# Kernel tuning notes

Measured on AMD Instinct MI355X. Metric: run time of the kernel, lower is better.

The kernel has to match this reference:

```python
import jax, jax.numpy as jnp
import numpy as np

B, H, L, N = 16, 256, 4096, 64  # N = d_state//2 retained complex-conjugate modes (S4D)
EPS = 1e-5


def setup_inputs() -> dict:
    key = jax.random.key(0)
    ks = jax.random.split(key, 6)
    x = jax.random.normal(ks[0], (B, H, L), dtype=jnp.float32)
    # dt log-uniform in [1e-3, 1e-1] per channel (standard S4 init)
    log_dt = (jax.random.uniform(ks[1], (H,), dtype=jnp.float32)
              * (np.log(0.1) - np.log(0.001)) + np.log(0.001))
    # S4D-Lin init: A_n = -1/2 + i*pi*n
    A_re = -0.5 * jnp.ones((H, N), dtype=jnp.float32)
    A_im = jnp.pi * jnp.broadcast_to(jnp.arange(N, dtype=jnp.float32), (H, N))
    # bidirectional -> 2 channel groups of C
    C_re = jax.random.normal(ks[2], (2, H, N), dtype=jnp.float32)
    C_im = jax.random.normal(ks[3], (2, H, N), dtype=jnp.float32)
    D = jax.random.normal(ks[4], (H,), dtype=jnp.float32)
    ln_w = jnp.ones((H,), dtype=jnp.float32)
    ln_b = jnp.zeros((H,), dtype=jnp.float32)
    W_out = jax.random.normal(ks[5], (H, H), dtype=jnp.float32) / np.sqrt(H)
    b_out = jnp.zeros((H,), dtype=jnp.float32)
    return {"x": x, "log_dt": log_dt, "A_re": A_re, "A_im": A_im,
            "C_re": C_re, "C_im": C_im, "D": D,
            "ln_w": ln_w, "ln_b": ln_b, "W_out": W_out, "b_out": b_out}


def _s4_forward(x, log_dt, A_re, A_im, C_re, C_im, D, ln_w, ln_b, W_out, b_out):
    # LayerNorm over channel dim (x.transpose -> LN(d_model) -> transpose back)
    mu = jnp.mean(x, axis=1, keepdims=True)
    var = jnp.mean((x - mu) ** 2, axis=1, keepdims=True)
    z = (x - mu) * jax.lax.rsqrt(var + EPS) * ln_w[None, :, None] + ln_b[None, :, None]

    # --- S4D kernel via Vandermonde (ZOH-style discretization) ---
    A = A_re + 1j * A_im                         # (H, N)
    C = C_re + 1j * C_im                         # (2, H, N)
    dt = jnp.exp(log_dt)[:, None]                # (H, 1)
    dtA = dt * A                                 # (H, N)
    C_t = C * (jnp.exp(dtA) - 1.0) / A           # (2, H, N)
    t = jnp.arange(L, dtype=jnp.float32)
    V = jnp.exp(dtA[:, :, None] * t)             # (H, N, L) Vandermonde
    K = 2.0 * jnp.real(jnp.einsum('dhn,hnl->dhl', C_t, V))  # (2, H, L)

    # bidirectional: forward kernel padded right, backward kernel flipped, padded left
    k = jnp.pad(K[0], ((0, 0), (0, L))) + jnp.pad(K[1][:, ::-1], ((0, 0), (L, 0)))

    # FFT convolution over length 2L
    Uf = jnp.fft.rfft(z, n=2 * L)                # (B, H, L+1)
    Kf = jnp.fft.rfft(k, n=2 * L)                # (H, L+1)
    y = jnp.fft.irfft(Uf * Kf[None], n=2 * L)[..., :L]

    y = y + D[None, :, None] * z                 # skip D*u
    y = jax.nn.gelu(y)                           # S4 default activation
    # transposed position-wise output linear (postact=None -> plain Linear)
    y = jnp.einsum('oh,bhl->bol', W_out, y) + b_out[None, :, None]
    return x + y                                  # residual


def reference(x, log_dt, A_re, A_im, C_re, C_im, D, ln_w, ln_b, W_out, b_out):
    return _s4_forward(x, log_dt, A_re, A_im, C_re, C_im, D, ln_w, ln_b, W_out, b_out)
```

## Files before the change

kernel.cpp:

```cpp
#include <hip/hip_runtime.h>
#include <math.h>

#define B_ 16
#define H_ 256
#define L_ 4096
#define N_ 64
#define HN (H_*N_)
#define HL (H_*L_)
#define BHL (B_*H_*L_)
#define SPAD 64

#define WVT_OFS 0
#define TM_OFS  8192
#define E2T_OFS 12288
#define MATS_PER 20480

typedef short bf16x8 __attribute__((ext_vector_type(8)));
typedef float f32x4  __attribute__((ext_vector_type(4)));

__device__ __forceinline__ unsigned int pk2(float a, float b) {
    return ((__float_as_uint(a) + 0x8000u) >> 16) |
           ((__float_as_uint(b) + 0x8000u) & 0xffff0000u);
}
__device__ __forceinline__ unsigned short bfr(float a) {
    return (unsigned short)((__float_as_uint(a) + 0x8000u) >> 16);
}
__device__ __forceinline__ float ubf(unsigned short u) {
    return __uint_as_float(((unsigned int)u) << 16);
}

__global__ void __launch_bounds__(64) mats_kernel(const float* __restrict__ log_dt,
                                                  const float* __restrict__ A_re,
                                                  const float* __restrict__ A_im,
                                                  const float* __restrict__ C_re,
                                                  const float* __restrict__ C_im,
                                                  unsigned short* __restrict__ mats,
                                                  float2* __restrict__ Wc) {
    int hd = blockIdx.x;
    int h = hd >> 1, d = hd & 1;
    int m = threadIdx.x;
    __shared__ float2 pws[65 * 64];
    __shared__ float2 c2s[64];
    __shared__ float  Karr[64];

    int i = h * 64 + m;
    float dt = expf(log_dt[h]);
    float Are = A_re[i], Aim = A_im[i];
    float dr = dt * Are, di = dt * Aim;
    float er = expf(dr);
    float wr = er * cosf(di), wi = er * sinf(di);
    float em1r = wr - 1.0f, em1i = wi;
    float inv = 1.0f / (Are * Are + Aim * Aim);
    float qr = (em1r * Are + em1i * Aim) * inv;
    float qi = (em1i * Are - em1r * Aim) * inv;
    float Cr = C_re[d * HN + i], Ci = C_im[d * HN + i];
    float2 c2;
    c2.x = 2.0f * (Cr * qr - Ci * qi);
    c2.y = 2.0f * (Cr * qi + Ci * qr);
    c2s[m] = c2;
    float pr = 1.0f, pi = 0.0f;
    for (int k = 0; k < 64; ++k) {
        float2 p; p.x = pr; p.y = pi;
        pws[k * 64 + ((m + k) & 63)] = p;
        float t = pr * wr - pi * wi;
        pi = pr * wi + pi * wr;
        pr = t;
    }
    {
        float2 p; p.x = pr; p.y = pi;
        pws[64 * 64 + ((m + 64) & 63)] = p;
        Wc[hd * 64 + m] = p;
    }
    __syncthreads();
    {
        float kk = 0.f;
        for (int mm = 0; mm < 64; ++mm) {
            float2 c = c2s[mm];
            float2 pw = pws[m * 64 + ((mm + m) & 63)];
            kk += c.x * pw.x - c.y * pw.y;
        }
        Karr[m] = kk;
    }
    __syncthreads();
    unsigned short* mb = mats + (size_t)hd * MATS_PER;
    for (int i2 = 0; i2 < 32; ++i2) {
        int e0 = 2 * i2, e1 = e0 + 1;
        int k0 = d ? e0 : 63 - e0;
        int k1 = d ? e1 : 63 - e1;
        float2 p0 = pws[k0 * 64 + ((m + k0) & 63)];
        float2 p1 = pws[k1 * 64 + ((m + k1) & 63)];
        *(unsigned int*)(mb + WVT_OFS + (2 * m) * 64 + e0)     = pk2(p0.x, p1.x);
        *(unsigned int*)(mb + WVT_OFS + (2 * m + 1) * 64 + e0) = pk2(p0.y, p1.y);
    }
    for (int i2 = 0; i2 < 32; ++i2) {
        int e0 = 2 * i2, e1 = e0 + 1;
        float v0, v1;
        if (d == 0) {
            v0 = (e0 <= m) ? Karr[m - e0] : 0.f;
            v1 = (e1 <= m) ? Karr[m - e1] : 0.f;
        } else {
            v0 = (e0 > m) ? Karr[e0 - m - 1] : 0.f;
            v1 = (e1 > m) ? Karr[e1 - m - 1] : 0.f;
        }
        *(unsigned int*)(mb + TM_OFS + m * 64 + e0) = pk2(v0, v1);
    }
    {
        int kp = d ? (63 - m) : (m + 1);
        for (int mm = 0; mm < 64; ++mm) {
            float2 c = c2s[mm];
            float2 pw = pws[kp * 64 + ((mm + kp) & 63)];
            float vr = c.x * pw.x - c.y * pw.y;
            float vi = -(c.x * pw.y + c.y * pw.x);
            *(unsigned int*)(mb + E2T_OFS + m * 128 + 2 * mm) = pk2(vr, vi);
        }
    }
}

__global__ void __launch_bounds__(256) wbf_kernel(const float* __restrict__ W,
                                                  unsigned short* __restrict__ Wbf) {
    int i = (blockIdx.x * 256 + threadIdx.x) * 4;
    float4 v = *(const float4*)(W + i);
    uint2 u;
    u.x = pk2(v.x, v.y);
    u.y = pk2(v.z, v.w);
    *(uint2*)(Wbf + i) = u;
}

__global__ void __launch_bounds__(256) ln_kernel(const float* __restrict__ x,
                                                 const float* __restrict__ lnw,
                                                 const float* __restrict__ lnb,
                                                 unsigned short* __restrict__ zb) {
    int b  = blockIdx.y;
    int l0 = blockIdx.x * 256;
    int t  = threadIdx.x;
    int hq = t >> 6, lo = t & 63;
    int l  = l0 + lo * 4;
    __shared__ float4 r1[4][64];
    __shared__ float4 r2[4][64];
    __shared__ float4 muS[64];
    __shared__ float4 rsS[64];
    const float* xb = x + (size_t)b * HL;
    float4 s1 = {0.f,0.f,0.f,0.f}, s2 = {0.f,0.f,0.f,0.f};
    #pragma unroll 4
    for (int hh = 0; hh < 64; ++hh) {
        int h = hq * 64 + hh;
        float4 v = *(const float4*)(xb + (size_t)h * L_ + l);
        s1.x += v.x; s1.y += v.y; s1.z += v.z; s1.w += v.w;
        s2.x += v.x*v.x; s2.y += v.y*v.y; s2.z += v.z*v.z; s2.w += v.w*v.w;
    }
    r1[hq][lo] = s1; r2[hq][lo] = s2;
    __syncthreads();
    if (t < 64) {
        float4 S1 = r1[0][t], S2 = r2[0][t];
        #pragma unroll
        for (int q = 1; q < 4; ++q) {
            float4 a = r1[q][t], c = r2[q][t];
            S1.x += a.x; S1.y += a.y; S1.z += a.z; S1.w += a.w;
            S2.x += c.x; S2.y += c.y; S2.z += c.z; S2.w += c.w;
        }
        const float invH = 1.0f / 256.0f;
        float4 mu, rs;
        mu.x = S1.x*invH; mu.y = S1.y*invH; mu.z = S1.z*invH; mu.w = S1.w*invH;
        rs.x = rsqrtf(S2.x*invH - mu.x*mu.x + 1e-5f);
        rs.y = rsqrtf(S2.y*invH - mu.y*mu.y + 1e-5f);
        rs.z = rsqrtf(S2.z*invH - mu.z*mu.z + 1e-5f);
        rs.w = rsqrtf(S2.w*invH - mu.w*mu.w + 1e-5f);
        muS[t] = mu; rsS[t] = rs;
    }
    __syncthreads();
    float4 mu = muS[lo], rs = rsS[lo];
    #pragma unroll 4
    for (int hh = 0; hh < 64; ++hh) {
        int h = hq * 64 + hh;
        float w = lnw[h], bb = lnb[h];
        float4 v = *(const float4*)(xb + (size_t)h * L_ + l);
        float4 zz;
        zz.x = (v.x - mu.x) * rs.x * w + bb;
        zz.y = (v.y - mu.y) * rs.y * w + bb;
        zz.z = (v.z - mu.z) * rs.z * w + bb;
        zz.w = (v.w - mu.w) * rs.w * w + bb;
        uint2 u;
        u.x = pk2(zz.x, zz.y);
        u.y = pk2(zz.z, zz.w);
        *(uint2*)(zb + (size_t)b * HL + (size_t)h * L_ + l) = u;
    }
}

#define MFMA16(a,b,c) __builtin_amdgcn_mfma_f32_16x16x32_bf16((a),(b),(c),0,0,0)
#define SU_BASE 8192

__global__ void __launch_bounds__(128, 3) ssm_kernel(const unsigned short* __restrict__ zb,
                                                     const unsigned short* __restrict__ mats,
                                                     const float2* __restrict__ Wc,
                                                     const float* __restrict__ D,
                                                     unsigned short* __restrict__ y2) {
    int bhd = blockIdx.x;
    int d  = bhd & 1;
    int bh = bhd >> 1;
    int h  = bh & (H_ - 1);
    int t  = threadIdx.x;
    int w  = t >> 6, l = t & 63;
    int p  = w;

    __shared__ __align__(16) char smem[24576];

    const unsigned short* mb = mats + (size_t)(h * 2 + d) * MATS_PER;

    {
        const char* zrow = (const char*)(zb + (size_t)bh * L_);
        #pragma unroll
        for (int k = 0; k < 4; ++k) {
            int row = w * 32 + k * 8 + (l >> 3);
            int chunk = (l & 7) ^ (row & 7);
            const char* src = zrow + row * 128 + chunk * 16;
            __builtin_amdgcn_global_load_lds(
                (const __attribute__((address_space(1))) unsigned int*)src,
                (__attribute__((address_space(3))) unsigned int*)(smem + w * 4096 + k * 1024),
                16, 0, 0);
        }
    }
    __syncthreads();

    bf16x8 za[4][2];
    int arow = l & 15;
    int koff = (l >> 4) * 8;
    #pragma unroll
    for (int cb = 0; cb < 4; ++cb) {
        int row = cb * 16 + arow;
        unsigned int sw = (row & 7) << 4;
        #pragma unroll
        for (int kb = 0; kb < 2; ++kb) {
            unsigned int byte = (unsigned)(row * 128 + (kb * 32 + koff) * 2) ^ sw;
            za[cb][kb] = *(bf16x8*)(smem + byte);
        }
    }

    char* sUd = smem + SU_BASE;
    #pragma unroll
    for (int mcb = 0; mcb < 4; ++mcb) {
        int mcblk = p * 4 + mcb;
        const unsigned short* wv = mb + WVT_OFS + (mcblk * 16 + arow) * 64 + koff;
        bf16x8 b0 = *(const bf16x8*)(wv);
        bf16x8 b1 = *(const bf16x8*)(wv + 32);
        #pragma unroll
        for (int cb = 0; cb < 4; ++cb) {
            f32x4 acc = {0.f, 0.f, 0.f, 0.f};
            acc = MFMA16(za[cb][0], b0, acc);
            acc = MFMA16(za[cb][1], b1, acc);
            int mc = mcblk * 16 + arow;
            #pragma unroll
            for (int rr = 0; rr < 4; ++rr) {
                int c = cb * 16 + (l >> 4) * 4 + rr;
                unsigned int byte = ((unsigned)(c * 256 + mc * 2)) ^ ((c & 7) << 4);
                *(unsigned short*)(sUd + byte) = bfr(acc[rr]);
            }
        }
    }
    __syncthreads();

    if (p == 0) {
        float2 w64 = Wc[(h * 2 + d) * 64 + l];
        float sr = 0.f, si = 0.f;
        if (d == 0) {
            for (int c = 0; c < 64; ++c) {
                unsigned int byte = ((unsigned)(c * 256 + l * 4)) ^ ((c & 7) << 4);
                unsigned int uu = *(unsigned int*)(sUd + byte);
                float ur = __uint_as_float(uu << 16);
                float ui = __uint_as_float(uu & 0xffff0000u);
                *(unsigned int*)(sUd + byte) = pk2(sr, si);
                float nsr = fmaf(w64.x, sr, fmaf(-w64.y, si, ur));
                float nsi = fmaf(w64.x, si, fmaf(w64.y, sr, ui));
                sr = nsr; si = nsi;
            }
        } else {
            for (int c = 63; c >= 0; --c) {
                unsigned int byte = ((unsigned)(c * 256 + l * 4)) ^ ((c & 7) << 4);
                unsigned int uu = *(unsigned int*)(sUd + byte);
                float ur = __uint_as_float(uu << 16);
                float ui = __uint_as_float(uu & 0xffff0000u);
                *(unsigned int*)(sUd + byte) = pk2(sr, si);
                float nsr = fmaf(w64.x, sr, fmaf(-w64.y, si, ur));
                float nsi = fmaf(w64.x, si, fmaf(w64.y, sr, ui));
                sr = nsr; si = nsi;
            }
        }
    }
    __syncthreads();

    f32x4 yacc[2][4];
    #pragma unroll
    for (int jb = 0; jb < 2; ++jb) {
        int jblk = p * 2 + jb;
        const unsigned short* tm = mb + TM_OFS + (jblk * 16 + arow) * 64 + koff;
        bf16x8 tb0 = *(const bf16x8*)(tm);
        bf16x8 tb1 = *(const bf16x8*)(tm + 32);
        const unsigned short* et = mb + E2T_OFS + (jblk * 16 + arow) * 128 + koff;
        bf16x8 eb0 = *(const bf16x8*)(et);
        bf16x8 eb1 = *(const bf16x8*)(et + 32);
        bf16x8 eb2 = *(const bf16x8*)(et + 64);
        bf16x8 eb3 = *(const bf16x8*)(et + 96);
        #pragma unroll
        for (int cb = 0; cb < 4; ++cb) {
            f32x4 acc = {0.f, 0.f, 0.f, 0.f};
            acc = MFMA16(za[cb][0], tb0, acc);
            acc = MFMA16(za[cb][1], tb1, acc);
            int row = cb * 16 + arow;
            unsigned int sw = (row & 7) << 4;
            bf16x8 sa0 = *(bf16x8*)(sUd + (((unsigned)(row * 256 + (0 * 32 + koff) * 2)) ^ sw));
            bf16x8 sa1 = *(bf16x8*)(sUd + (((unsigned)(row * 256 + (1 * 32 + koff) * 2)) ^ sw));
            bf16x8 sa2 = *(bf16x8*)(sUd + (((unsigned)(row * 256 + (2 * 32 + koff) * 2)) ^ sw));
            bf16x8 sa3 = *(bf16x8*)(sUd + (((unsigned)(row * 256 + (3 * 32 + koff) * 2)) ^ sw));
            acc = MFMA16(sa0, eb0, acc);
            acc = MFMA16(sa1, eb1, acc);
            acc = MFMA16(sa2, eb2, acc);
            acc = MFMA16(sa3, eb3, acc);
            yacc[jb][cb] = acc;
        }
    }
    __syncthreads();

    {
        float dv = D[h];
        #pragma unroll
        for (int jb = 0; jb < 2; ++jb) {
            int j = (p * 2 + jb) * 16 + arow;
            #pragma unroll
            for (int cb = 0; cb < 4; ++cb) {
                #pragma unroll
                for (int rr = 0; rr < 4; ++rr) {
                    int c = cb * 16 + (l >> 4) * 4 + rr;
                    unsigned int byte = ((unsigned)(c * 128 + j * 2)) ^ ((c & 7) << 4);
                    float val = yacc[jb][cb][rr];
                    if (d == 0) val += dv * ubf(*(unsigned short*)(smem + byte));
                    *(unsigned short*)(smem + byte) = bfr(val);
                }
            }
        }
    }
    __syncthreads();
    {
        int row = t >> 1, halfq = t & 1;
        unsigned int rsw = (row & 7) << 4;
        char* go = (char*)(y2 + ((size_t)bh * 2 + d) * L_);
        #pragma unroll
        for (int j = 0; j < 4; ++j) {
            unsigned int off = (unsigned)(row * 128 + halfq * 64 + j * 16);
            uint4 a = *(const uint4*)(smem + (off ^ rsw));
            *(uint4*)(go + off) = a;
        }
    }
}

__global__ void __launch_bounds__(256, 4) gt_kernel(const unsigned short* __restrict__ y2,
                                                    unsigned short* __restrict__ gT) {
    int b  = blockIdx.y;
    int l0 = blockIdx.x * 64;
    int t  = threadIdx.x;
    __shared__ __align__(16) char lT[64 * 512];
    size_t rbase = ((size_t)b * H_ + t) * 2 * L_ + l0;
    const uint4* yfp = (const uint4*)(y2 + rbase);
    const uint4* ybp = (const uint4*)(y2 + rbase + L_);
    #pragma unroll
    for (int j8 = 0; j8 < 8; ++j8) {
        uint4 a = yfp[j8];
        uint4 c = ybp[j8];
        #pragma unroll
        for (int e = 0; e < 8; ++e) {
            int l = j8 * 8 + e;
            float y = ubf(((const unsigned short*)&a)[e]) + ubf(((const unsigned short*)&c)[e]);
            float inner = 0.7978845608028654f * (y + 0.044715f * y * y * y);
            float en = __expf(-2.0f * inner);
            float g = y * __builtin_amdgcn_rcpf(1.0f + en);
            *(unsigned short*)(lT + (((unsigned)(l * 512 + t * 2)) ^ ((l & 7) << 4))) = bfr(g);
        }
    }
    __syncthreads();
    int l = t >> 2, seg = t & 3;
    unsigned short* dst = gT + ((size_t)b * L_ + l0 + l) * 256 + seg * 64;
    unsigned int sw = (l & 7) << 4;
    #pragma unroll
    for (int j = 0; j < 8; ++j) {
        uint4 u = *(const uint4*)(lT + (((unsigned)(l * 512 + seg * 128 + j * 16)) ^ sw));
        *(uint4*)(dst + j * 8) = u;
    }
}

__global__ void __launch_bounds__(256, 3) outproj_kernel(
        const unsigned short* __restrict__ gT,
        const unsigned short* __restrict__ Wbf,
        const float* __restrict__ x,
        const float* __restrict__ bias,
        float* __restrict__ out) {
    int b  = blockIdx.z;
    int o0 = blockIdx.y * 128;
    int l0 = blockIdx.x * 128;
    int t  = threadIdx.x;
    int w  = t >> 6, lane = t & 63;
    int wr = w >> 1, wc = w & 1;
    int l15 = lane & 15, q = lane >> 4;

    __shared__ __align__(16) char lds[34816];
    unsigned short* At = (unsigned short*)lds;
    unsigned short* Bt = (unsigned short*)(lds + 16384);

    f32x4 acc[4][4];
    #pragma unroll
    for (int i = 0; i < 4; ++i)
        #pragma unroll
        for (int j = 0; j < 4; ++j) acc[i][j] = (f32x4){0.f, 0.f, 0.f, 0.f};

    const unsigned short* gTb = gT + ((size_t)b * L_ + l0) * 256;
    const unsigned short* Wb0 = Wbf + (size_t)o0 * 256;
    unsigned int swz = (unsigned)(l15 & 7) << 4;

    for (int kt = 0; kt < 4; ++kt) {
        int k0 = kt * 64;
        #pragma unroll
        for (int s = 0; s < 4; ++s) {
            int id = (w * 4 + s) * 64 + lane;
            int row = id >> 3, ch = id & 7;
            int chl = ch ^ (row & 7);
            uint4 va = *(const uint4*)(gTb + (size_t)row * 256 + k0 + chl * 8);
            uint4 vb = *(const uint4*)(Wb0 + (size_t)row * 256 + k0 + chl * 8);
            *(uint4*)(At + id * 8) = va;
            *(uint4*)(Bt + id * 8) = vb;
        }
        __syncthreads();
        #pragma unroll
        for (int kk = 0; kk < 2; ++kk) {
            bf16x8 af[4], bfr_[4];
            #pragma unroll
            for (int rb = 0; rb < 4; ++rb) {
                int li = wr * 64 + rb * 16 + l15;
                af[rb] = *(const bf16x8*)((char*)At + li * 128 + (((kk * 64 + q * 16)) ^ swz));
                int oi = wc * 64 + rb * 16 + l15;
                bfr_[rb] = *(const bf16x8*)((char*)Bt + oi * 128 + (((kk * 64 + q * 16)) ^ swz));
            }
            #pragma unroll
            for (int rb = 0; rb < 4; ++rb)
                #pragma unroll
                for (int cb = 0; cb < 4; ++cb)
                    acc[rb][cb] = MFMA16(af[rb], bfr_[cb], acc[rb][cb]);
        }
        __syncthreads();
    }

    float* Eb = (float*)lds;
    for (int pp = 0; pp < 2; ++pp) {
        if (wc == pp) {
            #pragma unroll
            for (int cb = 0; cb < 4; ++cb) {
                int o_loc = cb * 16 + l15;
                unsigned int esw = (unsigned)(o_loc & 7) << 4;
                #pragma unroll
                for (int rb = 0; rb < 4; ++rb) {
                    int colbase = wr * 64 + rb * 16 + q * 4;
                    #pragma unroll
                    for (int r = 0; r < 4; ++r) {
                        int col = colbase + r;
                        *(float*)((char*)Eb + o_loc * 528 + (((unsigned)(col * 4)) ^ esw)) =
                            acc[rb][cb][r];
                    }
                }
            }
        }
        __syncthreads();
        int o_loc = t >> 2, lseg = t & 3;
        int o = o0 + pp * 64 + o_loc;
        float bo = bias[o];
        unsigned int esw = (unsigned)(o_loc & 7) << 4;
        size_t off = ((size_t)b * H_ + o) * L_ + l0 + lseg * 32;
        const float* xr = x + off;
        float* orow = out + off;
        #pragma unroll
        for (int j = 0; j < 8; ++j) {
            float4 e = *(const float4*)((char*)Eb + o_loc * 528 +
                                        (((unsigned)(lseg * 128 + j * 16)) ^ esw));
            float4 xv = *(const float4*)(xr + j * 4);
            float4 ov;
            ov.x = xv.x + bo + e.x;
            ov.y = xv.y + bo + e.y;
            ov.z = xv.z + bo + e.z;
            ov.w = xv.w + bo + e.w;
            *(float4*)(orow + j * 4) = ov;
        }
        __syncthreads();
    }
}

extern "C" void kernel_launch(void* const* d_in, const int* in_sizes, int n_in,
                              void* d_out, int out_size, void* d_ws, size_t ws_size,
                              hipStream_t stream) {
    const float* x      = (const float*)d_in[0];
    const float* log_dt = (const float*)d_in[1];
    const float* A_re   = (const float*)d_in[2];
    const float* A_im   = (const float*)d_in[3];
    const float* C_re   = (const float*)d_in[4];
    const float* C_im   = (const float*)d_in[5];
    const float* D      = (const float*)d_in[6];
    const float* lnw    = (const float*)d_in[7];
    const float* lnb    = (const float*)d_in[8];
    const float* W      = (const float*)d_in[9];
    const float* bout   = (const float*)d_in[10];
    float* out = (float*)d_out;

    unsigned short* zb   = (unsigned short*)d_ws;
    unsigned short* y2   = zb + (size_t)BHL + SPAD;
    unsigned short* gT   = y2 + 2 * (size_t)BHL + SPAD;
    unsigned short* mats = gT + (size_t)BHL + SPAD;
    float2* Wc = (float2*)(mats + 512 * (size_t)MATS_PER);
    unsigned short* Wbf = (unsigned short*)(Wc + 512 * 64);

    mats_kernel<<<512, 64, 0, stream>>>(log_dt, A_re, A_im, C_re, C_im, mats, Wc);
    wbf_kernel<<<64, 256, 0, stream>>>(W, Wbf);
    ln_kernel<<<dim3(L_ / 256, B_), 256, 0, stream>>>(x, lnw, lnb, zb);
    ssm_kernel<<<B_ * H_ * 2, 128, 0, stream>>>(zb, mats, Wc, D, y2);
    gt_kernel<<<dim3(L_ / 64, B_), 256, 0, stream>>>(y2, gT);
    outproj_kernel<<<dim3(L_ / 128, H_ / 128, B_), 256, 0, stream>>>(gT, Wbf, x, bout, out);
}
```

Before: 222.4 us.

## Fuse GELU and transpose into output projection GEMM tile loading

Removes the separate gt_kernel that applied GELU to the summed bidirectional outputs and wrote a transposed bf16 buffer. The outproj kernel now reads y2 directly, sums forward and backward halves, applies GELU and writes the transposed tile into LDS. This saves the intermediate write/read and a launch. In exchange, y2 is re-read and GELU recomputed for each of the two output-channel blocks, and the LDS stores become scattered 2-byte writes.

```diff
diff --git a/kernel.cpp b/kernel.cpp
--- a/kernel.cpp
+++ b/kernel.cpp
@@ -351,42 +351,8 @@
     }
 }
 
-__global__ void __launch_bounds__(256, 4) gt_kernel(const unsigned short* __restrict__ y2,
-                                                    unsigned short* __restrict__ gT) {
-    int b  = blockIdx.y;
-    int l0 = blockIdx.x * 64;
-    int t  = threadIdx.x;
-    __shared__ __align__(16) char lT[64 * 512];
-    size_t rbase = ((size_t)b * H_ + t) * 2 * L_ + l0;
-    const uint4* yfp = (const uint4*)(y2 + rbase);
-    const uint4* ybp = (const uint4*)(y2 + rbase + L_);
-    #pragma unroll
-    for (int j8 = 0; j8 < 8; ++j8) {
-        uint4 a = yfp[j8];
-        uint4 c = ybp[j8];
-        #pragma unroll
-        for (int e = 0; e < 8; ++e) {
-            int l = j8 * 8 + e;
-            float y = ubf(((const unsigned short*)&a)[e]) + ubf(((const unsigned short*)&c)[e]);
-            float inner = 0.7978845608028654f * (y + 0.044715f * y * y * y);
-            float en = __expf(-2.0f * inner);
-            float g = y * __builtin_amdgcn_rcpf(1.0f + en);
-            *(unsigned short*)(lT + (((unsigned)(l * 512 + t * 2)) ^ ((l & 7) << 4))) = bfr(g);
-        }
-    }
-    __syncthreads();
-    int l = t >> 2, seg = t & 3;
-    unsigned short* dst = gT + ((size_t)b * L_ + l0 + l) * 256 + seg * 64;
-    unsigned int sw = (l & 7) << 4;
-    #pragma unroll
-    for (int j = 0; j < 8; ++j) {
-        uint4 u = *(const uint4*)(lT + (((unsigned)(l * 512 + seg * 128 + j * 16)) ^ sw));
-        *(uint4*)(dst + j * 8) = u;
-    }
-}
-
 __global__ void __launch_bounds__(256, 3) outproj_kernel(
-        const unsigned short* __restrict__ gT,
+        const unsigned short* __restrict__ y2,
         const unsigned short* __restrict__ Wbf,
         const float* __restrict__ x,
         const float* __restrict__ bias,
@@ -409,20 +375,42 @@
         #pragma unroll
         for (int j = 0; j < 4; ++j) acc[i][j] = (f32x4){0.f, 0.f, 0.f, 0.f};
 
-    const unsigned short* gTb = gT + ((size_t)b * L_ + l0) * 256;
     const unsigned short* Wb0 = Wbf + (size_t)o0 * 256;
     unsigned int swz = (unsigned)(l15 & 7) << 4;
 
+    int h_loc = t >> 2, lq = t & 3;
+
     for (int kt = 0; kt < 4; ++kt) {
         int k0 = kt * 64;
+        {
+            const unsigned short* yb0 =
+                y2 + (((size_t)b * H_ + k0 + h_loc) * 2) * L_ + l0 + lq * 32;
+            uint4 f[4], g[4];
+            #pragma unroll
+            for (int j = 0; j < 4; ++j) f[j] = *(const uint4*)(yb0 + j * 8);
+            #pragma unroll
+            for (int j = 0; j < 4; ++j) g[j] = *(const uint4*)(yb0 + L_ + j * 8);
+            #pragma unroll
+            for (int j = 0; j < 4; ++j) {
+                #pragma unroll
+                for (int e = 0; e < 8; ++e) {
+                    int l_loc = lq * 32 + j * 8 + e;
+                    float y = ubf(((const unsigned short*)&f[j])[e]) +
+                              ubf(((const unsigned short*)&g[j])[e]);
+                    float inner = 0.7978845608028654f * (y + 0.044715f * y * y * y);
+                    float en = __expf(-2.0f * inner);
+                    float gv = y * __builtin_amdgcn_rcpf(1.0f + en);
+                    *(unsigned short*)((char*)At +
+                        (((unsigned)(l_loc * 128 + h_loc * 2)) ^ ((l_loc & 7) << 4))) = bfr(gv);
+                }
+            }
+        }
         #pragma unroll
         for (int s = 0; s < 4; ++s) {
             int id = (w * 4 + s) * 64 + lane;
             int row = id >> 3, ch = id & 7;
             int chl = ch ^ (row & 7);
-            uint4 va = *(const uint4*)(gTb + (size_t)row * 256 + k0 + chl * 8);
             uint4 vb = *(const uint4*)(Wb0 + (size_t)row * 256 + k0 + chl * 8);
-            *(uint4*)(At + id * 8) = va;
             *(uint4*)(Bt + id * 8) = vb;
         }
         __syncthreads();
@@ -506,8 +494,7 @@
 
     unsigned short* zb   = (unsigned short*)d_ws;
     unsigned short* y2   = zb + (size_t)BHL + SPAD;
-    unsigned short* gT   = y2 + 2 * (size_t)BHL + SPAD;
-    unsigned short* mats = gT + (size_t)BHL + SPAD;
+    unsigned short* mats = y2 + 2 * (size_t)BHL + SPAD;
     float2* Wc = (float2*)(mats + 512 * (size_t)MATS_PER);
     unsigned short* Wbf = (unsigned short*)(Wc + 512 * 64);
 
@@ -515,6 +502,5 @@
     wbf_kernel<<<64, 256, 0, stream>>>(W, Wbf);
     ln_kernel<<<dim3(L_ / 256, B_), 256, 0, stream>>>(x, lnw, lnb, zb);
     ssm_kernel<<<B_ * H_ * 2, 128, 0, stream>>>(zb, mats, Wc, D, y2);
-    gt_kernel<<<dim3(L_ / 64, B_), 256, 0, stream>>>(y2, gT);
-    outproj_kernel<<<dim3(L_ / 128, H_ / 128, B_), 256, 0, stream>>>(gT, Wbf, x, bout, out);
-}
+    outproj_kernel<<<dim3(L_ / 128, H_ / 128, B_), 256, 0, stream>>>(y2, Wbf, x, bout, out);
+}
```

Result: faster. 189.6 us (-14.7%).
